# Kernel optimization log

Measured on AMD Instinct MI355X. Metric: run time of the kernel, lower is better.

Reference implementation:

```python
import jax, jax.numpy as jnp
import numpy as np

NUM_HEADS = 16
HEAD_DIM = 128
SEQ_LEN = 2048
MAX_SEQ_LEN = 2048
NUM_PATTERNS = 4
BATCH = 4


def setup_inputs() -> dict:
    key = jax.random.key(0)
    ks = jax.random.split(key, 8)
    Q = jax.random.normal(ks[0], (BATCH, NUM_HEADS, SEQ_LEN, HEAD_DIM), dtype=jnp.float32)
    K = jax.random.normal(ks[1], (BATCH, NUM_HEADS, SEQ_LEN, HEAD_DIM), dtype=jnp.float32)
    V = jax.random.normal(ks[2], (BATCH, NUM_HEADS, SEQ_LEN, HEAD_DIM), dtype=jnp.float32)
    # SparseAttentionLearner params
    pattern_masks = jax.random.normal(ks[3], (NUM_PATTERNS, MAX_SEQ_LEN, MAX_SEQ_LEN), dtype=jnp.float32) * 0.1
    # pattern_selector: Linear(3,32) -> ReLU -> Linear(32,num_patterns)
    sel_w1 = jax.random.normal(ks[4], (3, 32), dtype=jnp.float32) * (1.0 / np.sqrt(3.0))
    sel_b1 = jax.random.normal(ks[5], (32,), dtype=jnp.float32) * 0.1
    sel_w2 = jax.random.normal(ks[6], (32, NUM_PATTERNS), dtype=jnp.float32) * (1.0 / np.sqrt(32.0))
    sel_b2 = jax.random.normal(ks[7], (NUM_PATTERNS,), dtype=jnp.float32) * 0.1
    return {"Q": Q, "K": K, "V": V, "pattern_masks": pattern_masks,
            "sel_w1": sel_w1, "sel_b1": sel_b1, "sel_w2": sel_w2, "sel_b2": sel_b2}


def reference(Q, K, V, pattern_masks, sel_w1, sel_b1, sel_w2, sel_b2):
    B, H, S, D = Q.shape
    # Per-head pattern-selector features: [seq_len/max_seq_len, head_id/12, 0.5]
    head_ids = jnp.arange(H, dtype=jnp.float32)
    feats = jnp.stack([
        jnp.full((H,), S / float(MAX_SEQ_LEN), dtype=jnp.float32),
        head_ids / 12.0,
        jnp.full((H,), 0.5, dtype=jnp.float32),
    ], axis=-1)  # [H, 3]
    hidden = jax.nn.relu(feats @ sel_w1 + sel_b1)          # [H, 32]
    logits = hidden @ sel_w2 + sel_b2                       # [H, num_patterns]
    pat_idx = jnp.argmax(logits, axis=-1)                   # [H]
    # Learned binary sparse masks per head: sigmoid > 0.5
    sel_masks = jnp.take(pattern_masks, pat_idx, axis=0)[:, :S, :S]  # [H, S, S]
    binary_mask = (jax.nn.sigmoid(sel_masks) > 0.5).astype(Q.dtype)   # [H, S, S]
    # Sparse attention: scores multiplied (not masked_fill) by binary mask
    scores = jnp.einsum('bhsd,bhtd->bhst', Q, K) / jnp.sqrt(jnp.float32(D)).astype(Q.dtype)
    scores = scores * binary_mask[None]
    attn = jax.nn.softmax(scores, axis=-1)
    out = jnp.einsum('bhst,bhtd->bhsd', attn, V)
    return out
```

## Files before the change

kernel.cpp:

```cpp
#include <hip/hip_runtime.h>
#include <hip/hip_bf16.h>
#include <math.h>

#define BATCH 4
#define NHEADS 16
#define SEQ 2048
#define HDIM 128
#define NPAT 4

#define BM 128
#define BN 64
#define NTHREADS 256
#define NKT (SEQ / BN)
#define TILE_BYTES 16384
#define NBLOCKS (BATCH * NHEADS * (SEQ / BM))

typedef _Float16 f16x8 __attribute__((ext_vector_type(8)));
typedef _Float16 f16x4 __attribute__((ext_vector_type(4)));
typedef float floatx4 __attribute__((ext_vector_type(4)));

typedef const __attribute__((address_space(1))) void gvoid_t;
typedef __attribute__((address_space(3))) void lvoid_t;

#if __has_builtin(__builtin_amdgcn_exp2f)
#define EXP2(x) __builtin_amdgcn_exp2f(x)
#else
#define EXP2(x) exp2f(x)
#endif

__global__ void sel_kernel(const float* __restrict__ w1, const float* __restrict__ b1,
                           const float* __restrict__ w2, const float* __restrict__ b2,
                           int* __restrict__ pat_idx, int* __restrict__ used) {
  int h = threadIdx.x;
  if (h < NPAT) used[h] = 0;
  __syncthreads();
  if (h >= NHEADS) return;
  float f0 = 1.0f;
  float f1 = (float)h / 12.0f;
  float f2 = 0.5f;
  float acc[NPAT] = {b2[0], b2[1], b2[2], b2[3]};
  for (int j = 0; j < 32; ++j) {
    float hj = f0 * w1[j] + f1 * w1[32 + j] + f2 * w1[64 + j] + b1[j];
    hj = fmaxf(hj, 0.0f);
    for (int p = 0; p < NPAT; ++p) acc[p] += hj * w2[j * NPAT + p];
  }
  int best = 0;
  float bv = acc[0];
  for (int p = 1; p < NPAT; ++p) {
    if (acc[p] > bv) { bv = acc[p]; best = p; }
  }
  pat_idx[h] = best;
  atomicOr(&used[best], 1);
}

__device__ __attribute__((noinline)) bool sig_gt_half_slow(float x) {
  float t = (float)exp(-(double)x);
  float s = 1.0f / (1.0f + t);
  return s > 0.5f;
}

__global__ void bin_kernel(const float* __restrict__ pm, unsigned int* __restrict__ bits,
                           const int* __restrict__ used) {
  int pat = blockIdx.x >> 9;
  if (!used[pat]) return;
  int t = blockIdx.x * blockDim.x + threadIdx.x;
  const float4* s4 = (const float4*)(pm + (size_t)t * 32);
  unsigned int w = 0;
  bool anyneed = false;
#pragma unroll
  for (int i = 0; i < 8; ++i) {
    float4 v = s4[i];
    float e[4] = {v.x, v.y, v.z, v.w};
#pragma unroll
    for (int j = 0; j < 4; ++j) {
      anyneed |= (fabsf(e[j]) < 1e-5f);
      w |= ((e[j] > 0.0f) ? 1u : 0u) << (i * 4 + j);
    }
  }
  if (__ballot(anyneed)) {
    if (anyneed) {
      w = 0;
#pragma unroll 1
      for (int i = 0; i < 8; ++i) {
        float4 v = s4[i];
        float e[4] = {v.x, v.y, v.z, v.w};
        for (int j = 0; j < 4; ++j) {
          bool b = (fabsf(e[j]) < 1e-5f) ? sig_gt_half_slow(e[j]) : (e[j] > 0.0f);
          w |= (b ? 1u : 0u) << (i * 4 + j);
        }
      }
    }
  }
  bits[t] = w;
}

__global__ __launch_bounds__(256) void prep_k(const float* __restrict__ K,
                                              _Float16* __restrict__ Kp) {
  size_t q0 = ((size_t)blockIdx.x * 256 + threadIdx.x) * 16;
  int tile = (int)(q0 >> 14);
  int p = (int)(q0 & 16383);
  int r = p >> 8;
  int cb = (p & 255) ^ ((r & 7) << 4);
  const float* src = K + ((size_t)tile * 64 + r) * HDIM + (cb >> 1);
  float4 a = ((const float4*)src)[0];
  float4 b = ((const float4*)src)[1];
  f16x8 f;
  f[0] = (_Float16)a.x; f[1] = (_Float16)a.y; f[2] = (_Float16)a.z; f[3] = (_Float16)a.w;
  f[4] = (_Float16)b.x; f[5] = (_Float16)b.y; f[6] = (_Float16)b.z; f[7] = (_Float16)b.w;
  *(f16x8*)((char*)Kp + q0) = f;
}

__global__ __launch_bounds__(256) void prep_vt(const float* __restrict__ V,
                                               _Float16* __restrict__ Vt) {
  __shared__ _Float16 tile[64][140];
  const int t = threadIdx.x;
  const float* vsrc = V + (size_t)blockIdx.x * 64 * HDIM;
#pragma unroll
  for (int i = 0; i < 8; ++i) {
    int idx = i * 256 + t;
    int kc = idx >> 5, c4 = idx & 31;
    float4 v = ((const float4*)(vsrc + kc * HDIM))[c4];
    f16x4 f;
    f[0] = (_Float16)v.x; f[1] = (_Float16)v.y; f[2] = (_Float16)v.z; f[3] = (_Float16)v.w;
    *(f16x4*)&tile[kc][c4 * 4] = f;
  }
  __syncthreads();
  char* dst = (char*)Vt + (size_t)blockIdx.x * TILE_BYTES;
#pragma unroll
  for (int i = 0; i < 4; ++i) {
    int p = (i * 256 + t) * 16;
    int d = p >> 7;
    int cp = (p & 127) >> 4;
    int clog = cp ^ (d & 7);
    int q = clog & 3, ks = clog >> 2;
    int T16 = ((q >> 1) * 2 + ks) << 4;
    f16x8 f;
#pragma unroll
    for (int j = 0; j < 8; ++j) {
      int qsel = (j < 4) ? q : (q ^ 2);
      int kc = T16 + qsel * 4 + (j & 3);
      f[j] = tile[kc][d];
    }
    *(f16x8*)(dst + p) = f;
  }
}

__global__ __launch_bounds__(NTHREADS, 2) void flash_kernel(
    const float* __restrict__ Q, const _Float16* __restrict__ Kp,
    const _Float16* __restrict__ Vt, const unsigned int* __restrict__ bits,
    const int* __restrict__ pat_idx, float* __restrict__ out) {
  __shared__ alignas(16) char kv_raw[2][2 * TILE_BYTES];
  __shared__ unsigned int maskw[2][BM][2];

  const int tid = threadIdx.x;
  const int wave = tid >> 6;
  const int lane = tid & 63;
  const int l16 = lane & 15;
  const int quad = lane >> 4;
  const int swz = l16 & 7;

  int bid = (int)blockIdx.x;
  bid = (bid & 7) * (NBLOCKS / 8) + (bid >> 3);
  const int bh = bid >> 4;
  const int qt = bid & 15;
  const int h = bh & (NHEADS - 1);
  const int qbase = qt * BM;
  const int pat = pat_idx[h];

  const float SCL = 0.08838834764831845f * 1.4426950408889634f;
  const float P_MIN = 6.103515625e-05f;

  const unsigned int* bits_p = bits + ((size_t)pat * SEQ + qbase) * (SEQ / 32);
  const char* kgbase = (const char*)Kp + (size_t)bh * NKT * TILE_BYTES + wave * 1024 + lane * 16;
  const char* vgbase = (const char*)Vt + (size_t)bh * NKT * TILE_BYTES + wave * 1024 + lane * 16;
  const unsigned int* mgbase = bits_p + (size_t)(wave * 32 + (lane >> 1)) * (SEQ / 32) + (lane & 1);

  auto stage = [&](int nb, int kt) {
    const char* kgt = kgbase + (size_t)kt * TILE_BYTES;
    const char* vgt = vgbase + (size_t)kt * TILE_BYTES;
    char* kl = &kv_raw[nb][0] + wave * 1024;
    char* vl = &kv_raw[nb][TILE_BYTES] + wave * 1024;
#pragma unroll
    for (int i = 0; i < 4; ++i) {
      __builtin_amdgcn_global_load_lds((gvoid_t*)(kgt + i * 4096),
                                       (lvoid_t*)(kl + i * 4096), 16, 0, 0);
      __builtin_amdgcn_global_load_lds((gvoid_t*)(vgt + i * 4096),
                                       (lvoid_t*)(vl + i * 4096), 16, 0, 0);
    }
    __builtin_amdgcn_global_load_lds((gvoid_t*)(mgbase + 2 * kt),
                                     (lvoid_t*)&maskw[nb][wave * 32][0], 4, 0, 0);
  };

  stage(0, 0);

  f16x8 qf[2][4];
#pragma unroll
  for (int mt = 0; mt < 2; ++mt) {
    const int row = qbase + wave * 32 + mt * 16 + l16;
    const float* qp = Q + ((size_t)bh * SEQ + row) * HDIM;
#pragma unroll
    for (int ks = 0; ks < 4; ++ks) {
      const float4* p4 = (const float4*)(qp + ks * 32 + quad * 8);
      float4 a = p4[0], c = p4[1];
      f16x8 f;
      f[0] = (_Float16)a.x; f[1] = (_Float16)a.y; f[2] = (_Float16)a.z; f[3] = (_Float16)a.w;
      f[4] = (_Float16)c.x; f[5] = (_Float16)c.y; f[6] = (_Float16)c.z; f[7] = (_Float16)c.w;
      qf[mt][ks] = f;
    }
  }

  floatx4 o_acc[2][8];
#pragma unroll
  for (int mt = 0; mt < 2; ++mt)
#pragma unroll
    for (int n = 0; n < 8; ++n) o_acc[mt][n] = (floatx4){0.f, 0.f, 0.f, 0.f};
  float m_run[2] = {-INFINITY, -INFINITY};
  float l_run[2] = {0.0f, 0.0f};

  __syncthreads();
  int cur = 0;

  for (int kt = 0; kt < NKT; ++kt) {
    if (kt + 1 < NKT) stage(cur ^ 1, kt + 1);

    const char* kbuf = &kv_raw[cur][0];
    const char* vbuf = &kv_raw[cur][TILE_BYTES];

    floatx4 sf[4][2];
#pragma unroll
    for (int t = 0; t < 4; ++t)
#pragma unroll
      for (int mt = 0; mt < 2; ++mt) sf[t][mt] = (floatx4){0.f, 0.f, 0.f, 0.f};
    __builtin_amdgcn_s_setprio(1);
#pragma unroll
    for (int t = 0; t < 4; ++t) {
      const char* krow = kbuf + ((t * 16 + l16) << 8);
#pragma unroll
      for (int ks = 0; ks < 4; ++ks) {
        f16x8 kf = *(const f16x8*)(krow + ((((ks << 2) | quad) ^ swz) << 4));
#pragma unroll
        for (int mt = 0; mt < 2; ++mt)
          sf[t][mt] = __builtin_amdgcn_mfma_f32_16x16x32_f16(kf, qf[mt][ks], sf[t][mt], 0, 0, 0);
      }
    }
    __builtin_amdgcn_s_setprio(0);

#pragma unroll
    for (int mt = 0; mt < 2; ++mt) {
      const int rl = wave * 32 + mt * 16 + l16;
      const unsigned w0 = maskw[cur][rl][0], w1 = maskw[cur][rl][1];
#pragma unroll
      for (int t = 0; t < 4; ++t) {
        const unsigned wd = (t & 2) ? w1 : w0;
        const int base = ((t & 1) << 4) + (quad << 2);
#pragma unroll
        for (int r = 0; r < 4; ++r) {
          float s = sf[t][mt][r];
          sf[t][mt][r] = ((wd >> (base + r)) & 1u) ? s * SCL : 0.0f;
        }
      }
    }
    float mx0 = sf[0][0][0], mx1 = sf[0][1][0];
#pragma unroll
    for (int t = 0; t < 4; ++t)
#pragma unroll
      for (int r = 0; r < 4; ++r) {
        mx0 = fmaxf(mx0, sf[t][0][r]);
        mx1 = fmaxf(mx1, sf[t][1][r]);
      }
    mx0 = fmaxf(mx0, __shfl_xor(mx0, 16));
    mx0 = fmaxf(mx0, __shfl_xor(mx0, 32));
    mx1 = fmaxf(mx1, __shfl_xor(mx1, 16));
    mx1 = fmaxf(mx1, __shfl_xor(mx1, 32));

    if (!__all((mx0 <= m_run[0]) && (mx1 <= m_run[1]))) {
      float alpha[2];
      const float mn0 = fmaxf(m_run[0], mx0);
      const float mn1 = fmaxf(m_run[1], mx1);
      alpha[0] = EXP2(m_run[0] - mn0);
      alpha[1] = EXP2(m_run[1] - mn1);
      m_run[0] = mn0; m_run[1] = mn1;
      l_run[0] *= alpha[0]; l_run[1] *= alpha[1];
#pragma unroll
      for (int mt = 0; mt < 2; ++mt) {
#pragma unroll
        for (int r = 0; r < 4; ++r) {
          const float ac = __shfl(alpha[mt], (quad << 2) | r, 16);
#pragma unroll
          for (int n = 0; n < 8; ++n) o_acc[mt][n][r] *= ac;
        }
      }
    }

    f16x4 hq[4][2];
#pragma unroll
    for (int mt = 0; mt < 2; ++mt) {
      const float mrow = m_run[mt];
      float ps = 0.0f;
#pragma unroll
      for (int t = 0; t < 4; ++t) {
#pragma unroll
        for (int r = 0; r < 4; ++r) {
          float p = EXP2(sf[t][mt][r] - mrow);
          if (p < P_MIN) p = 0.0f;
          _Float16 hh = (_Float16)p;
          hq[t][mt][r] = hh;
          ps += (float)hh;
        }
      }
      ps += __shfl_xor(ps, 16);
      ps += __shfl_xor(ps, 32);
      l_run[mt] += ps;
    }

    __builtin_amdgcn_s_setprio(1);
#pragma unroll
    for (int ks = 0; ks < 2; ++ks) {
      f16x8 pa[2];
#pragma unroll
      for (int mt = 0; mt < 2; ++mt) {
        f16x4 hk = (quad & 2) ? hq[ks + 2][mt] : hq[ks][mt];
        f16x4 hs = (quad & 2) ? hq[ks][mt] : hq[ks + 2][mt];
        union { f16x4 v; unsigned u[2]; } K_, S_;
        K_.v = hk; S_.v = hs;
        unsigned p0 = (unsigned)__shfl_xor((int)S_.u[0], 32);
        unsigned p1 = (unsigned)__shfl_xor((int)S_.u[1], 32);
        union { unsigned u[4]; f16x8 v; } P_;
        P_.u[0] = K_.u[0]; P_.u[1] = K_.u[1]; P_.u[2] = p0; P_.u[3] = p1;
        pa[mt] = P_.v;
      }
#pragma unroll
      for (int nt = 0; nt < 8; ++nt) {
        const char* vrow = vbuf + ((nt * 16 + l16) << 7);
        f16x8 vb = *(const f16x8*)(vrow + ((((ks << 2) | quad) ^ swz) << 4));
#pragma unroll
        for (int mt = 0; mt < 2; ++mt)
          o_acc[mt][nt] = __builtin_amdgcn_mfma_f32_16x16x32_f16(pa[mt], vb, o_acc[mt][nt], 0, 0, 0);
      }
    }
    __builtin_amdgcn_s_setprio(0);

    __syncthreads();
    cur ^= 1;
  }

#pragma unroll
  for (int mt = 0; mt < 2; ++mt) {
#pragma unroll
    for (int r = 0; r < 4; ++r) {
      const float lv = __shfl(l_run[mt], (quad << 2) | r, 16);
      const float inv = 1.0f / lv;
      const int row = qbase + wave * 32 + mt * 16 + quad * 4 + r;
      float* og = out + ((size_t)bh * SEQ + row) * HDIM + l16;
#pragma unroll
      for (int n = 0; n < 8; ++n) og[n * 16] = o_acc[mt][n][r] * inv;
    }
  }
}

extern "C" void kernel_launch(void* const* d_in, const int* in_sizes, int n_in,
                              void* d_out, int out_size, void* d_ws, size_t ws_size,
                              hipStream_t stream) {
  const float* Q  = (const float*)d_in[0];
  const float* K  = (const float*)d_in[1];
  const float* V  = (const float*)d_in[2];
  const float* pm = (const float*)d_in[3];
  const float* w1 = (const float*)d_in[4];
  const float* b1 = (const float*)d_in[5];
  const float* w2 = (const float*)d_in[6];
  const float* b2 = (const float*)d_in[7];
  float* out = (float*)d_out;

  int* pat_idx = (int*)d_ws;
  int* used = (int*)((char*)d_ws + 256);
  unsigned int* bits = (unsigned int*)((char*)d_ws + 4096);
  _Float16* Kp = (_Float16*)((char*)d_ws + 4096 + 2097152);
  _Float16* Vt = (_Float16*)((char*)d_ws + 4096 + 2097152 + 33554432);

  sel_kernel<<<1, 64, 0, stream>>>(w1, b1, w2, b2, pat_idx, used);
  bin_kernel<<<(NPAT * SEQ * (SEQ / 32)) / 256, 256, 0, stream>>>(pm, bits, used);
  prep_k<<<(BATCH * NHEADS * NKT * 1024) / 256, 256, 0, stream>>>(K, Kp);
  prep_vt<<<BATCH * NHEADS * NKT, 256, 0, stream>>>(V, Vt);
  flash_kernel<<<NBLOCKS, NTHREADS, 0, stream>>>(Q, Kp, Vt, bits, pat_idx, out);
}
```

Before: 479.3 us.

## Single-buffer K tile to cut LDS and raise occupancy to three blocks per CU

K now has one LDS buffer while V and the mask stay double-buffered. An extra barrier after the QK^T MFMAs lets the next K/V tiles be issued into the freed K slot during softmax and PV. This lowers LDS per block so launch bounds can ask for three blocks per CU. It also defers the cross-lane row-sum reduction of l to the end of the loop, which is valid because the rescaling is linear. The cost is an extra barrier per iteration, less overlap time for the K prefetch, and register pressure from the higher occupancy target, which may cause spills.

```diff
diff --git a/kernel.cpp b/kernel.cpp
--- a/kernel.cpp
+++ b/kernel.cpp
@@ -145,11 +145,12 @@
   }
 }
 
-__global__ __launch_bounds__(NTHREADS, 2) void flash_kernel(
+__global__ __launch_bounds__(NTHREADS, 3) void flash_kernel(
     const float* __restrict__ Q, const _Float16* __restrict__ Kp,
     const _Float16* __restrict__ Vt, const unsigned int* __restrict__ bits,
     const int* __restrict__ pat_idx, float* __restrict__ out) {
-  __shared__ alignas(16) char kv_raw[2][2 * TILE_BYTES];
+  __shared__ alignas(16) char kbuf_raw[TILE_BYTES];
+  __shared__ alignas(16) char vbuf_raw[2][TILE_BYTES];
   __shared__ unsigned int maskw[2][BM][2];
 
   const int tid = threadIdx.x;
@@ -175,23 +176,27 @@
   const char* vgbase = (const char*)Vt + (size_t)bh * NKT * TILE_BYTES + wave * 1024 + lane * 16;
   const unsigned int* mgbase = bits_p + (size_t)(wave * 32 + (lane >> 1)) * (SEQ / 32) + (lane & 1);
 
-  auto stage = [&](int nb, int kt) {
+  auto stage_k = [&](int kt) {
     const char* kgt = kgbase + (size_t)kt * TILE_BYTES;
-    const char* vgt = vgbase + (size_t)kt * TILE_BYTES;
-    char* kl = &kv_raw[nb][0] + wave * 1024;
-    char* vl = &kv_raw[nb][TILE_BYTES] + wave * 1024;
-#pragma unroll
-    for (int i = 0; i < 4; ++i) {
+    char* kl = kbuf_raw + wave * 1024;
+#pragma unroll
+    for (int i = 0; i < 4; ++i)
       __builtin_amdgcn_global_load_lds((gvoid_t*)(kgt + i * 4096),
                                        (lvoid_t*)(kl + i * 4096), 16, 0, 0);
+  };
+  auto stage_v = [&](int nb, int kt) {
+    const char* vgt = vgbase + (size_t)kt * TILE_BYTES;
+    char* vl = &vbuf_raw[nb][0] + wave * 1024;
+#pragma unroll
+    for (int i = 0; i < 4; ++i)
       __builtin_amdgcn_global_load_lds((gvoid_t*)(vgt + i * 4096),
                                        (lvoid_t*)(vl + i * 4096), 16, 0, 0);
-    }
     __builtin_amdgcn_global_load_lds((gvoid_t*)(mgbase + 2 * kt),
                                      (lvoid_t*)&maskw[nb][wave * 32][0], 4, 0, 0);
   };
 
-  stage(0, 0);
+  stage_k(0);
+  stage_v(0, 0);
 
   f16x8 qf[2][4];
 #pragma unroll
@@ -221,11 +226,6 @@
   int cur = 0;
 
   for (int kt = 0; kt < NKT; ++kt) {
-    if (kt + 1 < NKT) stage(cur ^ 1, kt + 1);
-
-    const char* kbuf = &kv_raw[cur][0];
-    const char* vbuf = &kv_raw[cur][TILE_BYTES];
-
     floatx4 sf[4][2];
 #pragma unroll
     for (int t = 0; t < 4; ++t)
@@ -234,7 +234,7 @@
     __builtin_amdgcn_s_setprio(1);
 #pragma unroll
     for (int t = 0; t < 4; ++t) {
-      const char* krow = kbuf + ((t * 16 + l16) << 8);
+      const char* krow = kbuf_raw + ((t * 16 + l16) << 8);
 #pragma unroll
       for (int ks = 0; ks < 4; ++ks) {
         f16x8 kf = *(const f16x8*)(krow + ((((ks << 2) | quad) ^ swz) << 4));
@@ -244,6 +244,13 @@
       }
     }
     __builtin_amdgcn_s_setprio(0);
+
+    __syncthreads();
+
+    if (kt + 1 < NKT) {
+      stage_k(kt + 1);
+      stage_v(cur ^ 1, kt + 1);
+    }
 
 #pragma unroll
     for (int mt = 0; mt < 2; ++mt) {
@@ -308,8 +315,6 @@
           ps += (float)hh;
         }
       }
-      ps += __shfl_xor(ps, 16);
-      ps += __shfl_xor(ps, 32);
       l_run[mt] += ps;
     }
 
@@ -331,7 +336,7 @@
       }
 #pragma unroll
       for (int nt = 0; nt < 8; ++nt) {
-        const char* vrow = vbuf + ((nt * 16 + l16) << 7);
+        const char* vrow = &vbuf_raw[cur][0] + ((nt * 16 + l16) << 7);
         f16x8 vb = *(const f16x8*)(vrow + ((((ks << 2) | quad) ^ swz) << 4));
 #pragma unroll
         for (int mt = 0; mt < 2; ++mt)
@@ -344,6 +349,11 @@
     cur ^= 1;
   }
 
+#pragma unroll
+  for (int mt = 0; mt < 2; ++mt) {
+    l_run[mt] += __shfl_xor(l_run[mt], 16);
+    l_run[mt] += __shfl_xor(l_run[mt], 32);
+  }
 #pragma unroll
   for (int mt = 0; mt < 2; ++mt) {
 #pragma unroll
```

Result: slower. 571.5 us (+19.2%).
